# Optimization experiments

Hardware: AMD Instinct MI355X
Metric: run time of the kernel (lower is better)

Reference implementation:

```python
import jax, jax.numpy as jnp
import numpy as np

L = 7  # window size (odd)
A = 0.1
B_COEF = 0.9


def mex_hat(d):
    grid = (np.mgrid[:d, :d] - d // 2) * 1.0
    eucl = (grid ** 2).sum(0) ** 0.5
    eucl /= d
    return eucl * np.exp(-eucl)


def setup_inputs() -> dict:
    key = jax.random.key(0)
    x = jax.random.normal(key, (16, 1, 512, 512), dtype=jnp.float32)
    kernel = jnp.asarray(mex_hat(L).reshape(-1), dtype=jnp.float32)  # [49], row-major like unfold
    return {"x": x, "kernel": kernel}


def reference(x, kernel):
    # x: [B,1,H,W], kernel: [L*L]
    # Extract zero-padded LxL patches, matching F.unfold(padding=L//2) ordering
    # (C=1, kernel positions row-major). patches: [B, L*L, H, W]
    patches = jax.lax.conv_general_dilated_patches(
        x, (L, L), (1, 1), 'SAME')
    average_term = jnp.exp(-patches.mean(axis=1, keepdims=True))  # [B,1,H,W]
    differential_term = jnp.sum(
        kernel[None, :, None, None] * jax.nn.relu(patches - x),
        axis=1, keepdims=True)  # [B,1,H,W]
    suppression = A * average_term + B_COEF * differential_term
    norm = jnp.sqrt(jnp.sum(suppression ** 2))
    suppression = suppression / norm
    mask = jnp.where(x > suppression, jnp.ones_like(x), jnp.zeros_like(x))
    return mask, average_term, differential_term
```

## Files before the change

kernel.cpp:

```cpp
#include <hip/hip_runtime.h>
#include <math.h>

#define HW 512
#define NB 16
#define TX 64
#define TY 64
#define LDSW 72
#define LDSH 70
#define N_PIX (NB * HW * HW)
#define NBLK (8 * 8 * NB)

__device__ __forceinline__ float sgpr_f(float v) {
    return __uint_as_float(__builtin_amdgcn_readfirstlane(__float_as_uint(v)));
}

__global__ __launch_bounds__(256, 4) void li_phase1(
    const float* __restrict__ x, const float* __restrict__ kw,
    float* __restrict__ out_ratio, float* __restrict__ out_avg,
    float* __restrict__ out_dif, float* __restrict__ partials)
{
    __shared__ float tile[LDSH * LDSW];
    __shared__ float wsum[4];

    const int tid = threadIdx.x;
    const int bx = blockIdx.x, by = blockIdx.y, b = blockIdx.z;
    const int x0 = bx * TX, y0 = by * TY;
    const float* xb = x + (size_t)b * (HW * HW);

    float w[49];
    float W = 0.f;
#pragma unroll
    for (int i = 0; i < 49; i++) { w[i] = sgpr_f(kw[i]); W += w[i]; }

    for (int idx = tid; idx < LDSH * (LDSW / 4); idx += 256) {
        int r = idx / (LDSW / 4);
        int c4 = idx - r * (LDSW / 4);
        int gy = y0 - 3 + r;
        int gx = x0 - 4 + c4 * 4;
        float4 v = make_float4(0.f, 0.f, 0.f, 0.f);
        if ((unsigned)gy < HW && (unsigned)gx < HW)
            v = *(const float4*)(xb + gy * HW + gx);
        *(float4*)&tile[r * LDSW + c4 * 4] = v;
    }
    __syncthreads();

    const int tx  = tid & 63;
    const int ty0 = (tid >> 6) * 16;

    float cen[16];
#pragma unroll
    for (int p = 0; p < 16; p++)
        cen[p] = tile[(ty0 + p + 3) * LDSW + tx + 4];

    float dif[16], bsum[16];
#pragma unroll
    for (int p = 0; p < 16; p++) { dif[p] = 0.f; bsum[p] = 0.f; }

    float vc[7], vn[7];
#pragma unroll
    for (int dj = 0; dj < 7; dj++)
        vc[dj] = tile[ty0 * LDSW + tx + 1 + dj];

#pragma unroll
    for (int r = 0; r < 22; r++) {
        if (r < 21) {
#pragma unroll
            for (int dj = 0; dj < 7; dj++)
                vn[dj] = tile[(ty0 + r + 1) * LDSW + tx + 1 + dj];
        }

        float rs = ((vc[0] + vc[1]) + (vc[2] + vc[3])) + ((vc[4] + vc[5]) + vc[6]);
#pragma unroll
        for (int p = 0; p < 16; p++) {
            const int di = r - p;
            if (di >= 0 && di < 7) {
                bsum[p] += rs;
#pragma unroll
                for (int dj = 0; dj < 7; dj++) {
                    if (di == 3 && dj == 3) continue;
                    dif[p] = fmaf(w[di * 7 + dj], fmaxf(vc[dj], cen[p]), dif[p]);
                }
            }
        }

#pragma unroll
        for (int dj = 0; dj < 7; dj++) vc[dj] = vn[dj];
    }

    const size_t base = (size_t)b * (HW * HW) + (size_t)(y0 + ty0) * HW + x0 + tx;
    float ss = 0.f;
#pragma unroll
    for (int p = 0; p < 16; p++) {
        float avg = __expf(-bsum[p] * (1.0f / 49.0f));
        float d = fmaf(-W, cen[p], dif[p]);
        float sp = 0.1f * avg + 0.9f * d;
        size_t gi = base + (size_t)p * HW;
        __builtin_nontemporal_store(avg, out_avg + gi);
        __builtin_nontemporal_store(d,   out_dif + gi);
        out_ratio[gi] = cen[p] * __builtin_amdgcn_rcpf(sp);
        ss = fmaf(sp, sp, ss);
    }

#pragma unroll
    for (int off = 32; off > 0; off >>= 1)
        ss += __shfl_down(ss, off, 64);
    if ((tid & 63) == 0) wsum[tid >> 6] = ss;
    __syncthreads();
    if (tid == 0)
        partials[bx + 8 * (by + 8 * b)] = (wsum[0] + wsum[1]) + (wsum[2] + wsum[3]);
}

__global__ __launch_bounds__(256) void li_phase2(
    const float* __restrict__ partials, float* __restrict__ io)
{
    __shared__ float wsum[4];
    __shared__ float s_inv;
    const int tid = threadIdx.x;

    float s = 0.f;
#pragma unroll
    for (int i = 0; i < NBLK / 256; i++)
        s += partials[tid + i * 256];
#pragma unroll
    for (int off = 32; off > 0; off >>= 1)
        s += __shfl_down(s, off, 64);
    if ((tid & 63) == 0) wsum[tid >> 6] = s;
    __syncthreads();
    if (tid == 0)
        s_inv = 1.0f / sqrtf((wsum[0] + wsum[1]) + (wsum[2] + wsum[3]));
    __syncthreads();

    const float inv = s_inv;
    const int base = blockIdx.x * 4096 + tid * 4;
#pragma unroll
    for (int k = 0; k < 4; k++) {
        const int i = base + k * 1024;
        float4 r = *(const float4*)(io + i);
        float4 m;
        m.x = (r.x > inv) ? 1.f : 0.f;
        m.y = (r.y > inv) ? 1.f : 0.f;
        m.z = (r.z > inv) ? 1.f : 0.f;
        m.w = (r.w > inv) ? 1.f : 0.f;
        *(float4*)(io + i) = m;
    }
}

extern "C" void kernel_launch(void* const* d_in, const int* in_sizes, int n_in,
                              void* d_out, int out_size, void* d_ws, size_t ws_size,
                              hipStream_t stream) {
    const float* x  = (const float*)d_in[0];
    const float* kw = (const float*)d_in[1];
    float* out   = (float*)d_out;
    float* ratio = out;
    float* avg   = out + N_PIX;
    float* dif   = out + 2 * (size_t)N_PIX;
    float* ws    = (float*)d_ws;

    dim3 g(HW / TX, HW / TY, NB);
    li_phase1<<<g, 256, 0, stream>>>(x, kw, ratio, avg, dif, ws);
    li_phase2<<<N_PIX / 4096, 256, 0, stream>>>(ws, ratio);
}
```

Baseline: 96.07 us.

## Compute 4x4 pixel micro-tiles per thread with vectorized LDS reads and stores

Each thread now computes a 4x4 block of output pixels instead of a 16x1 column strip. The stencil rows are read from LDS as float4 vectors, and horizontal box sums are updated with a sliding window. Results go to global memory as 128-bit vector stores. The aim is to cut LDS read traffic per pixel (10 rows of 12 values instead of 22 rows of 7 values per 16 pixels) and to cut the number of store instructions. The cost is more live registers, and the strided 4-wide accesses may cause LDS bank conflicts.

```diff
diff --git a/kernel.cpp b/kernel.cpp
--- a/kernel.cpp
+++ b/kernel.cpp
@@ -9,6 +9,8 @@
 #define LDSH 70
 #define N_PIX (NB * HW * HW)
 #define NBLK (8 * 8 * NB)
+
+using f32x4 = __attribute__((ext_vector_type(4))) float;
 
 __device__ __forceinline__ float sgpr_f(float v) {
     return __uint_as_float(__builtin_amdgcn_readfirstlane(__float_as_uint(v)));
@@ -44,61 +46,86 @@
     }
     __syncthreads();
 
-    const int tx  = tid & 63;
-    const int ty0 = (tid >> 6) * 16;
+    const int cx = tid & 15;
+    const int cy = tid >> 4;
+    const int colw = 4 * cx;
+    const int row0 = 4 * cy;
 
     float cen[16];
 #pragma unroll
-    for (int p = 0; p < 16; p++)
-        cen[p] = tile[(ty0 + p + 3) * LDSW + tx + 4];
+    for (int p = 0; p < 4; p++) {
+        float4 c4v = *(const float4*)&tile[(row0 + 3 + p) * LDSW + colw + 4];
+        cen[p*4+0] = c4v.x; cen[p*4+1] = c4v.y; cen[p*4+2] = c4v.z; cen[p*4+3] = c4v.w;
+    }
 
     float dif[16], bsum[16];
 #pragma unroll
-    for (int p = 0; p < 16; p++) { dif[p] = 0.f; bsum[p] = 0.f; }
+    for (int k = 0; k < 16; k++) { dif[k] = 0.f; bsum[k] = 0.f; }
 
-    float vc[7], vn[7];
-#pragma unroll
-    for (int dj = 0; dj < 7; dj++)
-        vc[dj] = tile[ty0 * LDSW + tx + 1 + dj];
+    float4 q0, q1, q2, n0, n1, n2;
+    {
+        const float* base = &tile[row0 * LDSW + colw];
+        q0 = *(const float4*)base;
+        q1 = *(const float4*)(base + 4);
+        q2 = *(const float4*)(base + 8);
+    }
 
 #pragma unroll
-    for (int r = 0; r < 22; r++) {
-        if (r < 21) {
+    for (int r = 0; r < 10; r++) {
+        if (r < 9) {
+            const float* base = &tile[(row0 + r + 1) * LDSW + colw];
+            n0 = *(const float4*)base;
+            n1 = *(const float4*)(base + 4);
+            n2 = *(const float4*)(base + 8);
+        }
+        float v[12] = {q0.x, q0.y, q0.z, q0.w,
+                       q1.x, q1.y, q1.z, q1.w,
+                       q2.x, q2.y, q2.z, q2.w};
+
+        float s0 = ((v[1] + v[2]) + (v[3] + v[4])) + ((v[5] + v[6]) + v[7]);
+        float s1 = s0 + (v[8]  - v[1]);
+        float s2 = s1 + (v[9]  - v[2]);
+        float s3 = s2 + (v[10] - v[3]);
+
 #pragma unroll
-            for (int dj = 0; dj < 7; dj++)
-                vn[dj] = tile[(ty0 + r + 1) * LDSW + tx + 1 + dj];
-        }
-
-        float rs = ((vc[0] + vc[1]) + (vc[2] + vc[3])) + ((vc[4] + vc[5]) + vc[6]);
+        for (int p = 0; p < 4; p++) {
+            const int di = r - p;
+            if (di < 0 || di >= 7) continue;
+            bsum[p*4+0] += s0; bsum[p*4+1] += s1;
+            bsum[p*4+2] += s2; bsum[p*4+3] += s3;
 #pragma unroll
-        for (int p = 0; p < 16; p++) {
-            const int di = r - p;
-            if (di >= 0 && di < 7) {
-                bsum[p] += rs;
+            for (int dj = 0; dj < 7; dj++) {
+                if (di == 3 && dj == 3) continue;
+                const float wv = w[di*7+dj];
 #pragma unroll
-                for (int dj = 0; dj < 7; dj++) {
-                    if (di == 3 && dj == 3) continue;
-                    dif[p] = fmaf(w[di * 7 + dj], fmaxf(vc[dj], cen[p]), dif[p]);
-                }
+                for (int j = 0; j < 4; j++)
+                    dif[p*4+j] = fmaf(wv, fmaxf(v[1+j+dj], cen[p*4+j]), dif[p*4+j]);
             }
         }
-
-#pragma unroll
-        for (int dj = 0; dj < 7; dj++) vc[dj] = vn[dj];
+        q0 = n0; q1 = n1; q2 = n2;
     }
 
-    const size_t base = (size_t)b * (HW * HW) + (size_t)(y0 + ty0) * HW + x0 + tx;
+    const size_t gbase = (size_t)b * (HW * HW) + (size_t)(y0 + row0) * HW + x0 + colw;
     float ss = 0.f;
 #pragma unroll
-    for (int p = 0; p < 16; p++) {
-        float avg = __expf(-bsum[p] * (1.0f / 49.0f));
-        float d = fmaf(-W, cen[p], dif[p]);
-        float sp = 0.1f * avg + 0.9f * d;
-        size_t gi = base + (size_t)p * HW;
-        __builtin_nontemporal_store(avg, out_avg + gi);
-        __builtin_nontemporal_store(d,   out_dif + gi);
-        out_ratio[gi] = cen[p] * __builtin_amdgcn_rcpf(sp);
-        ss = fmaf(sp, sp, ss);
+    for (int p = 0; p < 4; p++) {
+        float av[4], dv[4], rv[4];
+#pragma unroll
+        for (int j = 0; j < 4; j++) {
+            const int k = p*4+j;
+            av[j] = __expf(-bsum[k] * (1.0f / 49.0f));
+            dv[j] = fmaf(-W, cen[k], dif[k]);
+            const float spv = 0.1f * av[j] + 0.9f * dv[j];
+            rv[j] = cen[k] * __builtin_amdgcn_rcpf(spv);
+            ss = fmaf(spv, spv, ss);
+        }
+        const size_t gi = gbase + (size_t)p * HW;
+        f32x4 a4 = {av[0], av[1], av[2], av[3]};
+        f32x4 d4 = {dv[0], dv[1], dv[2], dv[3]};
+        f32x4 r4 = {rv[0], rv[1], rv[2], rv[3]};
+        __builtin_nontemporal_store(a4, (f32x4*)(out_avg + gi));
+        __builtin_nontemporal_store(d4, (f32x4*)(out_dif + gi));
+        *(f32x4*)(out_ratio + gi) = r4;
     }
 
 #pragma unroll
```

Result: slower. 118.5 us (+23.4%).
